# Performance work log

Measured on AMD Instinct MI355X. Metric: run time of the kernel, lower is better.

## Reference

```python
import jax, jax.numpy as jnp
import numpy as np

N, L, D, H = 2, 2048, 1024, 16
DK = D // H  # 64


def setup_inputs() -> dict:
    key = jax.random.key(0)
    ks = jax.random.split(key, 8)
    Xq = jax.random.normal(ks[0], (N, L, D), dtype=jnp.float32)
    Xk = jax.random.normal(ks[1], (N, L, D), dtype=jnp.float32)
    Xv = jax.random.normal(ks[2], (N, L, D), dtype=jnp.float32)
    mask_2d = jax.random.randint(ks[3], (N, L, L), 0, 2, dtype=jnp.int32)
    scale = 0.02
    Wq = jax.random.normal(ks[4], (D, D), dtype=jnp.float32) * scale
    Wk = jax.random.normal(ks[5], (D, D), dtype=jnp.float32) * scale
    Wv = jax.random.normal(ks[6], (D, D), dtype=jnp.float32) * scale
    Wo = jax.random.normal(ks[7], (D, D), dtype=jnp.float32) * scale
    return {"Xq": Xq, "Xk": Xk, "Xv": Xv, "Wq": Wq, "Wk": Wk, "Wv": Wv, "Wo": Wo, "mask_2d": mask_2d}


def reference(Xq, Xk, Xv, Wq, Wk, Wv, Wo, mask_2d):
    # Projections (bias=False). Per-head slicing in the original == reshape to [N,L,H,DK].
    Q = (Xq @ Wq).reshape(N, L, H, DK)
    K = (Xk @ Wk).reshape(N, L, H, DK)
    V = (Xv @ Wv).reshape(N, L, H, DK)
    # Scaled dot-product scores: [N, H, L, L]
    scores = jnp.einsum("blhd,bmhd->bhlm", Q, K) / jnp.sqrt(jnp.asarray(DK, scores_dtype(Q)))
    # NOTE: original uses masked_fill(mask==0, 0) BEFORE softmax (zero-fill, not -inf).
    scores = jnp.where(mask_2d[:, None, :, :] == 0, jnp.zeros((), scores.dtype), scores)
    A = jax.nn.softmax(scores, axis=-1)
    O = jnp.einsum("bhlm,bmhd->blhd", A, V).reshape(N, L, D)
    return O @ Wo


def scores_dtype(Q):
    return Q.dtype
```

## Files before the change

### kernel.cpp

```cpp
#include <hip/hip_runtime.h>
#include <hip/hip_bf16.h>

#define NB 2
#define L_SEQ 2048
#define NH 16
#define DKH 64
#define DMODEL 1024
#define MROWS (NB * L_SEQ)
#define QSCALE 0.18033688f
#define DD (DMODEL * DMODEL)

typedef __attribute__((ext_vector_type(8))) short short8;
typedef __attribute__((ext_vector_type(4))) float f32x4;

static __device__ __forceinline__ unsigned short f2bf(float f) {
    unsigned u = __float_as_uint(f);
    u += 0x7fffu + ((u >> 16) & 1u);
    return (unsigned short)(u >> 16);
}

static __device__ __forceinline__ float fexp2(float x) {
#if __has_builtin(__builtin_amdgcn_exp2f)
    return __builtin_amdgcn_exp2f(x);
#else
    return __expf(x * 0.6931471806f);
#endif
}

static __device__ __forceinline__ unsigned pk_bf16(float a, float b) {
    __hip_bfloat162 h = __float22bfloat162_rn(make_float2(a, b));
    return *reinterpret_cast<unsigned*>(&h);
}

static __device__ __forceinline__ void gll16(const void* g, void* l) {
    __builtin_amdgcn_global_load_lds(
        (const __attribute__((address_space(1))) void*)g,
        (__attribute__((address_space(3))) void*)l, 16, 0, 0);
}

__global__ __launch_bounds__(256)
void prep(const float* __restrict__ Xq, const float* __restrict__ Xk,
          const float* __restrict__ Xv, const float* __restrict__ w0,
          const float* __restrict__ w1, const float* __restrict__ w2,
          const float* __restrict__ w3, const int* __restrict__ mask,
          unsigned short* __restrict__ XB, unsigned short* __restrict__ WtB,
          unsigned long long* __restrict__ MWT)
{
    __shared__ float ts[32][33];
    const int bx = blockIdx.x;
    const int t  = threadIdx.x;

    if (bx < 12288) {
        const int z = bx >> 12;
        const float* src = (z == 0) ? Xq : (z == 1) ? Xk : Xv;
        const size_t i4 = (size_t)(bx & 4095) * 256 + t;
        float4 v = ((const float4*)src)[i4];
        ushort4 o;
        o.x = f2bf(v.x); o.y = f2bf(v.y); o.z = f2bf(v.z); o.w = f2bf(v.w);
        ((ushort4*)(XB + (size_t)z * 4194304))[i4] = o;
    } else if (bx < 16384) {
        const int idx = bx - 12288;
        const int z   = idx >> 10;
        const int rem = idx & 1023;
        const float* W = (z == 0) ? w0 : (z == 1) ? w1 : (z == 2) ? w2 : w3;
        unsigned short* Wt = WtB + (size_t)z * DD;
        const int n0 = (rem & 31) * 32;
        const int k0 = (rem >> 5) * 32;
        const int r  = t >> 3;
        const int c  = (t & 7) * 4;
        float4 v = *(const float4*)&W[(size_t)(k0 + r) * DMODEL + n0 + c];
        ts[r][c + 0] = v.x; ts[r][c + 1] = v.y;
        ts[r][c + 2] = v.z; ts[r][c + 3] = v.w;
        __syncthreads();
        ushort4 o;
        o.x = f2bf(ts[c + 0][r]); o.y = f2bf(ts[c + 1][r]);
        o.z = f2bf(ts[c + 2][r]); o.w = f2bf(ts[c + 3][r]);
        *(ushort4*)&Wt[(size_t)(n0 + r) * DMODEL + k0 + c] = o;
    } else {
        const int lane = t & 63;
        const size_t wbase = (size_t)(bx - 16384) * 4 + (t >> 6);
#pragma unroll
        for (int it = 0; it < 8; ++it) {
            const size_t wid = wbase + (size_t)it * 16384;
            const int mv = mask[wid * 64 + lane];
            const unsigned long long bits = __ballot(mv != 0);
            if (lane == 0) {
                const int b   = (int)(wid >> 16);
                const int rem = (int)(wid & 65535);
                const int row = rem >> 5;
                const int wd  = rem & 31;
                MWT[((size_t)b * 32 + wd) * L_SEQ + row] = bits;
            }
        }
    }
}

__global__ __launch_bounds__(256)
void gemm_qkv(const unsigned short* __restrict__ XB,
              const unsigned short* __restrict__ WtB,
              unsigned short* __restrict__ QKV)
{
    __shared__ __align__(16) unsigned short SMEM[16384];

    const int t    = threadIdx.x;
    const int w    = t >> 6;
    const int lane = t & 63;

    const int bid   = blockIdx.x;
    const int xcd   = bid & 7;
    const int idx   = bid >> 3;
    const int pair  = xcd * 12 + (idx >> 3);
    const int n0    = (idx & 7) * 128;
    const int m0    = (pair & 31) * 128;
    const int z     = pair >> 5;

    const unsigned short* A = XB  + (size_t)z * ((size_t)MROWS * DMODEL);
    const unsigned short* B = WtB + (size_t)z * DD;

    const int srow = lane >> 2;
    const int sc4  = (lane & 3) ^ (srow & 3);

    const unsigned short* ag[2];
    const unsigned short* bg[2];
    int lao[2], lbo[2];
#pragma unroll
    for (int g = 0; g < 2; ++g) {
        const int R = w * 32 + g * 16;
        ag[g] = A + (size_t)(m0 + R + srow) * DMODEL + sc4 * 8;
        bg[g] = B + (size_t)(n0 + R + srow) * DMODEL + sc4 * 8;
        lao[g] = R * 32;
        lbo[g] = R * 32;
    }

    const int ml = lane & 15;
    const int q  = lane >> 4;
    const int wm = (w >> 1) * 64;
    const int wn = (w & 1) * 64;

    const f32x4 z4 = {0.f, 0.f, 0.f, 0.f};
    f32x4 acc[4][4];
#pragma unroll
    for (int i = 0; i < 4; ++i)
#pragma unroll
        for (int j = 0; j < 4; ++j) acc[i][j] = z4;

#pragma unroll
    for (int g = 0; g < 2; ++g) {
        gll16(ag[g], &SMEM[lao[g]]);
        gll16(bg[g], &SMEM[8192 + lbo[g]]);
    }

    for (int j = 0; j < 32; ++j) {
        const int cur = j & 1;
        __syncthreads();
        if (j < 31) {
            const int kt = (j + 1) * 32;
            const int nb = (cur ^ 1) * 4096;
#pragma unroll
            for (int g = 0; g < 2; ++g) {
                gll16(ag[g] + kt, &SMEM[nb + lao[g]]);
                gll16(bg[g] + kt, &SMEM[8192 + nb + lbo[g]]);
            }
        }
        const unsigned short* As = &SMEM[cur * 4096];
        const unsigned short* Bs = &SMEM[8192 + cur * 4096];
        short8 av[4], bv[4];
#pragma unroll
        for (int mt = 0; mt < 4; ++mt)
            av[mt] = *(const short8*)
                &As[(wm + mt * 16 + ml) * 32 + ((q ^ (ml & 3)) * 8)];
#pragma unroll
        for (int nt = 0; nt < 4; ++nt)
            bv[nt] = *(const short8*)
                &Bs[(wn + nt * 16 + ml) * 32 + ((q ^ (ml & 3)) * 8)];
#pragma unroll
        for (int mt = 0; mt < 4; ++mt)
#pragma unroll
            for (int nt = 0; nt < 4; ++nt)
                acc[mt][nt] = __builtin_amdgcn_mfma_f32_16x16x32_bf16(
                    av[mt], bv[nt], acc[mt][nt], 0, 0, 0);
    }

    unsigned short* O = QKV + (size_t)z * ((size_t)MROWS * DMODEL);
    __syncthreads();
    unsigned short* Ts = SMEM;

    if (z == 2) {
#pragma unroll
        for (int mt = 0; mt < 4; ++mt) {
            const int trow0 = wm + mt * 16 + q * 4;
            const int ch    = trow0 >> 3;
#pragma unroll
            for (int nt = 0; nt < 4; ++nt) {
                const int tcol = wn + nt * 16 + ml;
                const int pc   = (ch & 8) | ((ch & 7) ^ (tcol & 7));
                ushort4 pv;
                pv.x = f2bf(acc[mt][nt][0]); pv.y = f2bf(acc[mt][nt][1]);
                pv.z = f2bf(acc[mt][nt][2]); pv.w = f2bf(acc[mt][nt][3]);
                *(ushort4*)&Ts[tcol * 128 + pc * 8 + (trow0 & 7)] = pv;
            }
        }
        __syncthreads();
        const int bb = m0 >> 11;
        const int l0 = (m0 & (L_SEQ - 1)) + (t & 15) * 8;
        const int cr = t & 15;
#pragma unroll
        for (int it = 0; it < 8; ++it) {
            const int tcol = (t >> 4) + 16 * it;
            const int pc   = (cr & 8) | ((cr & 7) ^ (tcol & 7));
            short8 vv = *(const short8*)&Ts[tcol * 128 + pc * 8];
            const int n  = n0 + tcol;
            const int hh = n >> 6;
            const int dk = n & (DKH - 1);
            *(short8*)&O[((size_t)(bb * NH + hh) * DKH + dk) * L_SEQ + l0] = vv;
        }
    } else {
        const float qs = (z == 0) ? QSCALE : 1.0f;
#pragma unroll
        for (int mt = 0; mt < 4; ++mt) {
            const int row0 = wm + mt * 16 + q * 4;
#pragma unroll
            for (int nt = 0; nt < 4; ++nt) {
                const int col = wn + nt * 16 + ml;
#pragma unroll
                for (int r = 0; r < 4; ++r)
                    Ts[(row0 + r) * 128 + col] = f2bf(acc[mt][nt][r] * qs);
            }
        }
        __syncthreads();
        const int mloc = t >> 3;
        const int c0   = t & 7;
#pragma unroll
        for (int pass = 0; pass < 4; ++pass) {
#pragma unroll
            for (int half = 0; half < 2; ++half) {
                const int m = mloc + 32 * pass;
                const int c = c0 + 8 * half;
                short8 v = *(const short8*)&Ts[m * 128 + c * 8];
                const int row = m0 + m;
                const int bb  = row >> 11;
                const int l   = row & (L_SEQ - 1);
                const int n   = n0 + c * 8;
                const int hh  = n >> 6;
                const int dk  = n & (DKH - 1);
                *(short8*)&O[(((size_t)(bb * NH + hh) * L_SEQ + l) << 6) + dk] = v;
            }
        }
    }
}

__global__ __launch_bounds__(256)
void gemm_out(const unsigned short* __restrict__ OB,
              const unsigned short* __restrict__ Wt,
              float* __restrict__ out)
{
    __shared__ __align__(16) unsigned short As[2][2048];
    __shared__ __align__(16) unsigned short Bs[2][4096];

    const int t    = threadIdx.x;
    const int w    = t >> 6;
    const int lane = t & 63;

    const int bid = blockIdx.x;
    const int xcd = bid & 7;
    const int idx = bid >> 3;
    const int n0  = (idx & 7) * 128;
    const int m0  = (xcd * 8 + (idx >> 3)) * 64;

    const int srow = lane >> 2;
    const int sc4  = (lane & 3) ^ (srow & 3);

    const unsigned short* ag =
        OB + (size_t)(m0 + w * 16 + srow) * DMODEL + sc4 * 8;
    const unsigned short* bg[2];
    int lbo[2];
#pragma unroll
    for (int g = 0; g < 2; ++g) {
        const int R = w * 32 + g * 16;
        bg[g] = Wt + (size_t)(n0 + R + srow) * DMODEL + sc4 * 8;
        lbo[g] = R * 32;
    }
    const int lao = (w * 16) * 32;

    const int ml = lane & 15;
    const int q  = lane >> 4;
    const int wm = (w >> 1) * 32;
    const int wn = (w & 1) * 64;

    const f32x4 z4 = {0.f, 0.f, 0.f, 0.f};
    f32x4 acc[2][4];
#pragma unroll
    for (int i = 0; i < 2; ++i)
#pragma unroll
        for (int j = 0; j < 4; ++j) acc[i][j] = z4;

    gll16(ag, &As[0][lao]);
#pragma unroll
    for (int g = 0; g < 2; ++g) gll16(bg[g], &Bs[0][lbo[g]]);

    for (int j = 0; j < 32; ++j) {
        const int cur = j & 1;
        __syncthreads();
        if (j < 31) {
            const int kt = (j + 1) * 32;
            gll16(ag + kt, &As[cur ^ 1][lao]);
#pragma unroll
            for (int g = 0; g < 2; ++g)
                gll16(bg[g] + kt, &Bs[cur ^ 1][lbo[g]]);
        }
        short8 av[2], bv[4];
#pragma unroll
        for (int mt = 0; mt < 2; ++mt)
            av[mt] = *(const short8*)
                &As[cur][(wm + mt * 16 + ml) * 32 + ((q ^ (ml & 3)) * 8)];
#pragma unroll
        for (int nt = 0; nt < 4; ++nt)
            bv[nt] = *(const short8*)
                &Bs[cur][(wn + nt * 16 + ml) * 32 + ((q ^ (ml & 3)) * 8)];
#pragma unroll
        for (int mt = 0; mt < 2; ++mt)
#pragma unroll
            for (int nt = 0; nt < 4; ++nt)
                acc[mt][nt] = __builtin_amdgcn_mfma_f32_16x16x32_bf16(
                    av[mt], bv[nt], acc[mt][nt], 0, 0, 0);
    }

#pragma unroll
    for (int mt = 0; mt < 2; ++mt) {
        const int gr0 = m0 + wm + mt * 16 + q * 4;
#pragma unroll
        for (int nt = 0; nt < 4; ++nt) {
            const int col = n0 + wn + nt * 16 + ml;
#pragma unroll
            for (int r = 0; r < 4; ++r)
                out[(size_t)(gr0 + r) * DMODEL + col] = acc[mt][nt][r];
        }
    }
}

__global__ __launch_bounds__(512, 4)
void attn_mfma(const unsigned short* __restrict__ Qb,
               const unsigned short* __restrict__ Kb,
               const unsigned short* __restrict__ Vtb,
               const unsigned long long* __restrict__ MWT,
               unsigned short* __restrict__ OB)
{
    __shared__ __align__(16) unsigned short Ks[2][64 * 64];
    __shared__ __align__(16) unsigned short Vts[2][64 * 64];
    __shared__ __align__(16) unsigned short Ps[8][16 * 64];
    __shared__ __align__(16) unsigned long long MskL[2][128];

    const int t    = threadIdx.x;
    const int w    = t >> 6;
    const int lane = t & 63;
    const int ml   = lane & 15;
    const int quad = lane >> 4;

    const int bid = blockIdx.x;
    const int xcd = bid & 7;
    const int idx = bid >> 3;
    const int p   = xcd * 4 + (idx >> 4);
    const int jq  = idx & 15;
    const int h   = p & 15;
    const int b   = p >> 4;
    const int q0  = jq * 128;

    const size_t hoff = (size_t)(b * NH + h) * L_SEQ * DKH;
    const unsigned short* Qh  = Qb  + hoff;
    const unsigned short* Kh  = Kb  + hoff;
    const unsigned short* Vth = Vtb + hoff;

    const int srow = lane >> 3;
    const int sc   = (lane & 7) ^ srow;

    unsigned short* QL = &Ks[0][0];
    gll16(Qh + (size_t)(q0 + w * 16 + srow) * DKH + sc * 8,
          &QL[(w * 16) * 64]);
    gll16(Qh + (size_t)(q0 + w * 16 + 8 + srow) * DKH + sc * 8,
          &QL[(w * 16 + 8) * 64]);

    const unsigned short* kg = Kh + (size_t)(w * 8 + srow) * DKH + sc * 8;
    const unsigned short* vg = Vth + (size_t)(w * 8 + srow) * L_SEQ + sc * 8;

    short8 kr = *(const short8*)kg;  kg += 64 * DKH;
    short8 vr = *(const short8*)vg;  vg += 64;

    const unsigned long long* mg = MWT + (size_t)b * 32 * L_SEQ + q0 + t;
    unsigned long long m_pf = 0;
    if (t < 128) m_pf = mg[0];

    __syncthreads();

    short8 qf[2];
#pragma unroll
    for (int s = 0; s < 2; ++s)
        qf[s] = *(const short8*)
            &QL[(w * 16 + ml) * 64 + (((s * 4 + quad) ^ (ml & 7)) * 8)];

    __syncthreads();

    *(short8*)&Ks[0][(w * 8) * 64 + lane * 8]  = kr;
    *(short8*)&Vts[0][(w * 8) * 64 + lane * 8] = vr;
    if (t < 128) MskL[0][t] = m_pf;

    kr = *(const short8*)kg;  kg += 64 * DKH;
    vr = *(const short8*)vg;  vg += 64;
    if (t < 128) m_pf = mg[L_SEQ];

    f32x4 oacc[4];
    const f32x4 z4 = {0.f, 0.f, 0.f, 0.f};
#pragma unroll
    for (int dt = 0; dt < 4; ++dt) oacc[dt] = z4;
    float l_i = 0.f;

    __syncthreads();

    for (int j = 0; j < 32; ++j) {
        const int cur = j & 1;
        if (j < 31) {
            const int nxt = cur ^ 1;
            *(short8*)&Ks[nxt][(w * 8) * 64 + lane * 8]  = kr;
            *(short8*)&Vts[nxt][(w * 8) * 64 + lane * 8] = vr;
            if (t < 128) MskL[nxt][t] = m_pf;
            if (j < 30) {
                kr = *(const short8*)kg;  kg += 64 * DKH;
                vr = *(const short8*)vg;  vg += 64;
                if (t < 128) m_pf = mg[(size_t)(j + 2) * L_SEQ];
            }
        }

        f32x4 sacc[4];
#pragma unroll
        for (int kt = 0; kt < 4; ++kt) sacc[kt] = z4;
#pragma unroll
        for (int s = 0; s < 2; ++s) {
            short8 kf[4];
#pragma unroll
            for (int kt = 0; kt < 4; ++kt)
                kf[kt] = *(const short8*)
                    &Ks[cur][(kt * 16 + ml) * 64 +
                             (((s * 4 + quad) ^ (ml & 7)) * 8)];
#pragma unroll
            for (int kt = 0; kt < 4; ++kt)
                sacc[kt] = __builtin_amdgcn_mfma_f32_16x16x32_bf16(
                    kf[kt], qf[s], sacc[kt], 0, 0, 0);
        }

        const unsigned long long wq = MskL[cur][w * 16 + ml] >> (quad * 4);
        const unsigned mlo = (unsigned)wq;
        const unsigned mhi = (unsigned)(wq >> 32);
        float rs = 0.f;
        float pr[4][4];
#pragma unroll
        for (int kt = 0; kt < 4; ++kt) {
            const unsigned word = (kt < 2) ? mlo : mhi;
            const int base = (kt & 1) * 16;
#pragma unroll
            for (int r = 0; r < 4; ++r) {
                const float mf = (float)((word >> (base + r)) & 1u);
                const float e  = fexp2(sacc[kt][r] * mf);
                pr[kt][r] = e;
                rs += e;
            }
        }
        rs += __shfl_xor(rs, 16);
        rs += __shfl_xor(rs, 32);
        l_i += rs;
#pragma unroll
        for (int kt = 0; kt < 4; ++kt) {
            uint2 pk;
            pk.x = pk_bf16(pr[kt][0], pr[kt][1]);
            pk.y = pk_bf16(pr[kt][2], pr[kt][3]);
            const int cp = (kt * 2 + (quad >> 1)) ^ (ml & 7);
            *(uint2*)&Ps[w][ml * 64 + cp * 8 + (quad & 1) * 4] = pk;
        }

#pragma unroll
        for (int s = 0; s < 2; ++s) {
            const short8 pf = *(const short8*)
                &Ps[w][ml * 64 + (((s * 4 + quad) ^ (ml & 7)) * 8)];
#pragma unroll
            for (int dt = 0; dt < 4; ++dt) {
                const short8 vf = *(const short8*)
                    &Vts[cur][(dt * 16 + ml) * 64 +
                              (((s * 4 + quad) ^ (ml & 7)) * 8)];
                oacc[dt] = __builtin_amdgcn_mfma_f32_16x16x32_bf16(
                    vf, pf, oacc[dt], 0, 0, 0);
            }
        }

        __syncthreads();
    }

    const float inv = 1.0f / l_i;
    const int qrow = q0 + w * 16 + ml;
#pragma unroll
    for (int dt = 0; dt < 4; ++dt) {
        ushort4 o4;
        o4.x = f2bf(oacc[dt][0] * inv);
        o4.y = f2bf(oacc[dt][1] * inv);
        o4.z = f2bf(oacc[dt][2] * inv);
        o4.w = f2bf(oacc[dt][3] * inv);
        *(ushort4*)&OB[(size_t)(b * L_SEQ + qrow) * DMODEL + h * DKH +
                       dt * 16 + quad * 4] = o4;
    }
}

extern "C" void kernel_launch(void* const* d_in, const int* in_sizes, int n_in,
                              void* d_out, int out_size, void* d_ws, size_t ws_size,
                              hipStream_t stream)
{
    (void)in_sizes; (void)n_in; (void)out_size; (void)ws_size;

    const float* Xq   = (const float*)d_in[0];
    const float* Xk   = (const float*)d_in[1];
    const float* Xv   = (const float*)d_in[2];
    const float* Wq   = (const float*)d_in[3];
    const float* Wk   = (const float*)d_in[4];
    const float* Wv   = (const float*)d_in[5];
    const float* Wo   = (const float*)d_in[6];
    const int*   mask = (const int*)d_in[7];
    float* out = (float*)d_out;

    char* base = (char*)d_ws;
    unsigned short*     XB  = (unsigned short*)base;
    unsigned short*     WtB = (unsigned short*)(base + (24u << 20));
    unsigned short*     QKV = (unsigned short*)(base + (32u << 20));
    unsigned short*     OB  = (unsigned short*)(base + (56u << 20));
    unsigned long long* MWT = (unsigned long long*)(base + (64u << 20));

    const size_t tsz = (size_t)MROWS * DMODEL;

    prep<<<dim3(20480), 256, 0, stream>>>(
        Xq, Xk, Xv, Wq, Wk, Wv, Wo, mask, XB, WtB, MWT);

    gemm_qkv<<<dim3(768), 256, 0, stream>>>(XB, WtB, QKV);

    attn_mfma<<<dim3(512), 512, 0, stream>>>(
        QKV, QKV + tsz, QKV + 2 * tsz, MWT, OB);

    gemm_out<<<dim3(512), 256, 0, stream>>>(OB, WtB + 3 * (size_t)DD, out);
}
```

Baseline: 247.8 us.

## Redistribute softmax probabilities via permlane swaps instead of LDS round-trip

Removes the per-wave Ps shared-memory buffer used to transpose the P tile from the QK^T MFMA output layout into the PV MFMA input layout. Instead, packed bf16 pairs are exchanged across lanes with permlane32/permlane16 swap builtins, falling back to shuffles when those builtins are unavailable. The mask application also switches from an int-to-float convert and multiply to a sign-extended bitfield AND on the score bits. This cuts LDS traffic and frees shared memory, but it relies on the lane permutation exactly matching the old swizzled layout.

```diff
diff --git a/kernel.cpp b/kernel.cpp
--- a/kernel.cpp
+++ b/kernel.cpp
@@ -12,6 +12,8 @@
 
 typedef __attribute__((ext_vector_type(8))) short short8;
 typedef __attribute__((ext_vector_type(4))) float f32x4;
+typedef __attribute__((ext_vector_type(2))) int int2v;
+typedef __attribute__((ext_vector_type(4))) int int4v;
 
 static __device__ __forceinline__ unsigned short f2bf(float f) {
     unsigned u = __float_as_uint(f);
@@ -36,6 +38,42 @@
     __builtin_amdgcn_global_load_lds(
         (const __attribute__((address_space(1))) void*)g,
         (__attribute__((address_space(3))) void*)l, 16, 0, 0);
+}
+
+static __device__ __forceinline__ int2v pl32swap(int a, int b) {
+#if __has_builtin(__builtin_amdgcn_permlane32_swap)
+    return __builtin_amdgcn_permlane32_swap(a, b, false, false);
+#else
+    const int pa = __shfl_xor(a, 32);
+    const int pb = __shfl_xor(b, 32);
+    const bool lo = ((threadIdx.x & 63) < 32);
+    int2v r;
+    r.x = lo ? a : pb;
+    r.y = lo ? pa : b;
+    return r;
+#endif
+}
+
+static __device__ __forceinline__ int2v pl16swap(int a, int b) {
+#if __has_builtin(__builtin_amdgcn_permlane16_swap)
+    return __builtin_amdgcn_permlane16_swap(a, b, false, false);
+#else
+    const int pa = __shfl_xor(a, 16);
+    const int pb = __shfl_xor(b, 16);
+    const bool ev = (((threadIdx.x >> 4) & 1) == 0);
+    int2v r;
+    r.x = ev ? a : pb;
+    r.y = ev ? pa : b;
+    return r;
+#endif
+}
+
+static __device__ __forceinline__ int sbfe1(int word, int off) {
+#if __has_builtin(__builtin_amdgcn_sbfe)
+    return __builtin_amdgcn_sbfe(word, off, 1);
+#else
+    return (word << (31 - off)) >> 31;
+#endif
 }
 
 __global__ __launch_bounds__(256)
@@ -347,7 +385,6 @@
 {
     __shared__ __align__(16) unsigned short Ks[2][64 * 64];
     __shared__ __align__(16) unsigned short Vts[2][64 * 64];
-    __shared__ __align__(16) unsigned short Ps[8][16 * 64];
     __shared__ __align__(16) unsigned long long MskL[2][128];
 
     const int t    = threadIdx.x;
@@ -453,12 +490,14 @@
         float pr[4][4];
 #pragma unroll
         for (int kt = 0; kt < 4; ++kt) {
-            const unsigned word = (kt < 2) ? mlo : mhi;
+            const int word = (int)((kt < 2) ? mlo : mhi);
             const int base = (kt & 1) * 16;
 #pragma unroll
             for (int r = 0; r < 4; ++r) {
-                const float mf = (float)((word >> (base + r)) & 1u);
-                const float e  = fexp2(sacc[kt][r] * mf);
+                const int mm = sbfe1(word, base + r);
+                const float sm =
+                    __int_as_float(__float_as_int(sacc[kt][r]) & mm);
+                const float e = fexp2(sm);
                 pr[kt][r] = e;
                 rs += e;
             }
@@ -466,19 +505,23 @@
         rs += __shfl_xor(rs, 16);
         rs += __shfl_xor(rs, 32);
         l_i += rs;
+
+        int p01[4], p23[4];
 #pragma unroll
         for (int kt = 0; kt < 4; ++kt) {
-            uint2 pk;
-            pk.x = pk_bf16(pr[kt][0], pr[kt][1]);
-            pk.y = pk_bf16(pr[kt][2], pr[kt][3]);
-            const int cp = (kt * 2 + (quad >> 1)) ^ (ml & 7);
-            *(uint2*)&Ps[w][ml * 64 + cp * 8 + (quad & 1) * 4] = pk;
+            p01[kt] = (int)pk_bf16(pr[kt][0], pr[kt][1]);
+            p23[kt] = (int)pk_bf16(pr[kt][2], pr[kt][3]);
         }
 
 #pragma unroll
         for (int s = 0; s < 2; ++s) {
-            const short8 pf = *(const short8*)
-                &Ps[w][ml * 64 + (((s * 4 + quad) ^ (ml & 7)) * 8)];
+            const int2v w01 = pl32swap(p01[2 * s], p01[2 * s + 1]);
+            const int2v r01 = pl16swap(w01.x, w01.y);
+            const int2v w23 = pl32swap(p23[2 * s], p23[2 * s + 1]);
+            const int2v r23 = pl16swap(w23.x, w23.y);
+            int4v pw;
+            pw.x = r01.x; pw.y = r23.x; pw.z = r01.y; pw.w = r23.y;
+            const short8 pf = __builtin_bit_cast(short8, pw);
 #pragma unroll
             for (int dt = 0; dt < 4; ++dt) {
                 const short8 vf = *(const short8*)
```

New measurement: 251.9 us. Within noise of the previous version (+1.7%).
